# Optimization experiments

Hardware: AMD Instinct MI355X
Metric: run time of the kernel (lower is better)

## Reference

```python
import jax, jax.numpy as jnp
import numpy as np

FT_IN = 40960   # HalfKP-style feature space
FFT_IN = 640    # factorized piece-square features
FT_OUT = 256


def setup_inputs() -> dict:
    key = jax.random.key(0)
    ks = jax.random.split(key, 10)
    B, A = 16384, 30  # batch, active features per board
    inp = {
        "stm_idx": jax.random.randint(ks[0], (B, A), 0, FT_IN, dtype=jnp.int32),
        "nstm_idx": jax.random.randint(ks[1], (B, A), 0, FT_IN, dtype=jnp.int32),
        "f_stm_idx": jax.random.randint(ks[2], (B, A), 0, FFT_IN, dtype=jnp.int32),
        "f_nstm_idx": jax.random.randint(ks[3], (B, A), 0, FFT_IN, dtype=jnp.int32),
        # learned parameters (glorot-ish scale)
        "ft_w": jax.random.normal(ks[4], (FT_IN, FT_OUT), jnp.float32) * 0.01,
        "ft_b": jax.random.normal(ks[5], (FT_OUT,), jnp.float32) * 0.01,
        "fft_w": jax.random.normal(ks[6], (FFT_IN, FT_OUT), jnp.float32) * 0.05,
        "fft_b": jax.random.normal(ks[7], (FT_OUT,), jnp.float32) * 0.01,
        "out_w": jax.random.normal(ks[8], (2 * FT_OUT, 1), jnp.float32) * 0.05,
        "out_b": jax.random.normal(ks[9], (1,), jnp.float32) * 0.01,
    }
    return inp


def _accumulate(w, b, idx):
    # sparse one-hot board @ kernel + bias == gather rows and sum over active features
    return jnp.take(w, idx, axis=0).sum(axis=1) + b  # [B, FT_OUT]


def reference(stm_idx, nstm_idx, f_stm_idx, f_nstm_idx,
              ft_w, ft_b, fft_w, fft_b, out_w, out_b):
    stm = _accumulate(ft_w, ft_b, stm_idx)        # [B, 256]
    nstm = _accumulate(ft_w, ft_b, nstm_idx)      # [B, 256]
    f_stm = _accumulate(fft_w, fft_b, f_stm_idx)  # [B, 256]
    f_nstm = _accumulate(fft_w, fft_b, f_nstm_idx)
    merge = jnp.concatenate((stm, nstm), axis=1) + jnp.concatenate((f_stm, f_nstm), axis=1)
    h = jnp.clip(merge, 0.0, 1.0)                 # ReLU(max_value=1.0)
    return jax.nn.sigmoid(h @ out_w + out_b)      # [B, 1]
```

## Files before the change

### kernel.cpp

```cpp
#include <hip/hip_runtime.h>
#include <math.h>

#define FT_IN  40960
#define FFT_IN 640
#define FT_OUT 256
#define NA     30
#define NSLICE 4
#define BPB    128

typedef _Float16 h2 __attribute__((ext_vector_type(2)));
typedef unsigned u32x4 __attribute__((ext_vector_type(4)));

__device__ __forceinline__ h2 u2h2(unsigned u) {
    union { unsigned u; h2 h; } c; c.u = u; return c.h;
}
__device__ __forceinline__ unsigned pkh(float a, float b) {
    union { h2 h; unsigned u; } c; c.h = h2{(_Float16)a, (_Float16)b}; return c.u;
}

__device__ __forceinline__ void conv_block(const float* __restrict__ src,
                                           unsigned* __restrict__ dst,
                                           int nrows, int bid, int tid)
{
    int t = bid * 256 + tid;
    int total = nrows * 32;
    if (t >= total) return;
    int r = t >> 5, g = t & 31;
    int s = g >> 3, d = g & 7;
    const float4* sp = (const float4*)(src + (size_t)r * FT_OUT + g * 8);
    float4 v0 = sp[0], v1 = sp[1];
    uint4 u;
    u.x = pkh(v0.x, v0.y); u.y = pkh(v0.z, v0.w);
    u.z = pkh(v1.x, v1.y); u.w = pkh(v1.z, v1.w);
    ((uint4*)dst)[((size_t)s * nrows + r) * 8 + d] = u;
}

__global__ __launch_bounds__(256) void prep(
    const float* __restrict__ ft_w, const float* __restrict__ fft_w,
    const int* __restrict__ stm, const int* __restrict__ nstm,
    const int* __restrict__ fstm, const int* __restrict__ fnstm,
    unsigned* __restrict__ ft_o, unsigned* __restrict__ fft_o,
    ushort4* __restrict__ pidx, int n_boards, int nb_ft, int nb_fft)
{
    int bid = blockIdx.x;
    if (bid < nb_ft) {
        conv_block(ft_w, ft_o, FT_IN, bid, threadIdx.x);
    } else if (bid < nb_ft + nb_fft) {
        conv_block(fft_w, fft_o, FFT_IN, bid - nb_ft, threadIdx.x);
    } else {
        int t = (bid - nb_ft - nb_fft) * 256 + (int)threadIdx.x;
        int total = n_boards * NA;
        if (t < total) {
            int board = t / NA, a = t - board * NA;
            ushort4 v;
            v.x = (unsigned short)stm[t];  v.y = (unsigned short)nstm[t];
            v.z = (unsigned short)fstm[t]; v.w = (unsigned short)fnstm[t];
            pidx[(size_t)a * n_boards + board] = v;
        }
    }
}

__global__ __launch_bounds__(1024, 4) void nnue_gather(
    const uint2* __restrict__ pidx,
    const char* __restrict__ ft, const char* __restrict__ fft,
    const float* __restrict__ ft_b, const float* __restrict__ fft_b,
    const float* __restrict__ out_w, float* __restrict__ partial, int n_boards)
{
    extern __shared__ char smem[];
    uint2* lidx = (uint2*)smem;
    u32x4* lfft = (u32x4*)(smem + NA * BPB * 8);
    const int slice = blockIdx.x & (NSLICE - 1);
    const int group = blockIdx.x >> 2;
    const int tid = (int)threadIdx.x;

    for (int i = tid; i < NA * BPB; i += 1024) {
        int b = i & (BPB - 1);
        int bd = group * BPB + b;
        uint2 v; v.x = 0u; v.y = 0u;
        if (bd < n_boards) v = pidx[(size_t)(i >> 7) * n_boards + bd];
        lidx[i] = v;
    }
    {
        const u32x4* fsrc = (const u32x4*)(fft + (size_t)slice * FFT_IN * 128);
        for (int i = tid; i < FFT_IN * 8; i += 1024)
            lfft[i] = fsrc[i];
    }
    __syncthreads();

    const int sub = tid >> 3, ql = tid & 7;
    int board = group * BPB + sub;
    const bool active = board < n_boards;
    const unsigned qlo = (unsigned)(ql << 4);
    const char* ftS = ft + (size_t)slice * FT_IN * 128 + qlo;
    const int col = slice * 64 + ql * 8;

    h2 z = h2{(_Float16)0.f, (_Float16)0.f};
    h2 a0[4] = {z, z, z, z};
    h2 a1[4] = {z, z, z, z};

    #pragma unroll
    for (int a = 0; a < NA; ++a) {
        uint2 iv = lidx[a * BPB + sub];
        u32x4 u0 = *(const u32x4*)(ftS + ((iv.x & 0xFFFFu) << 7));
        u32x4 u1 = *(const u32x4*)(ftS + ((iv.x >> 16) << 7));
        u32x4 g0 = lfft[((iv.y & 0xFFFFu) << 3) + ql];
        u32x4 g1 = lfft[((iv.y >> 16) << 3) + ql];
        a0[0] += u2h2(u0.x); a0[1] += u2h2(u0.y); a0[2] += u2h2(u0.z); a0[3] += u2h2(u0.w);
        a1[0] += u2h2(u1.x); a1[1] += u2h2(u1.y); a1[2] += u2h2(u1.z); a1[3] += u2h2(u1.w);
        a0[0] += u2h2(g0.x); a0[1] += u2h2(g0.y); a0[2] += u2h2(g0.z); a0[3] += u2h2(g0.w);
        a1[0] += u2h2(g1.x); a1[1] += u2h2(g1.y); a1[2] += u2h2(g1.z); a1[3] += u2h2(g1.w);
    }

    float h0[8], h1[8];
    #pragma unroll
    for (int i = 0; i < 4; ++i) {
        h0[2*i] = (float)a0[i].x; h0[2*i+1] = (float)a0[i].y;
        h1[2*i] = (float)a1[i].x; h1[2*i+1] = (float)a1[i].y;
    }
    const float4* bfp = (const float4*)(ft_b  + col);
    const float4* bgp = (const float4*)(fft_b + col);
    float4 bf0 = bfp[0], bf1 = bfp[1], bg0 = bgp[0], bg1 = bgp[1];
    float bias[8] = {bf0.x+bg0.x, bf0.y+bg0.y, bf0.z+bg0.z, bf0.w+bg0.w,
                     bf1.x+bg1.x, bf1.y+bg1.y, bf1.z+bg1.z, bf1.w+bg1.w};
    const float4* w0p = (const float4*)(out_w + col);
    const float4* w1p = (const float4*)(out_w + FT_OUT + col);
    float4 w00 = w0p[0], w01 = w0p[1], w10 = w1p[0], w11 = w1p[1];
    float w0[8] = {w00.x, w00.y, w00.z, w00.w, w01.x, w01.y, w01.z, w01.w};
    float w1[8] = {w10.x, w10.y, w10.z, w10.w, w11.x, w11.y, w11.z, w11.w};

    float p = 0.f;
    #pragma unroll
    for (int i = 0; i < 8; ++i) {
        p += fminf(fmaxf(h0[i] + bias[i], 0.f), 1.f) * w0[i];
        p += fminf(fmaxf(h1[i] + bias[i], 0.f), 1.f) * w1[i];
    }
    p += __shfl_xor(p, 1, 64);
    p += __shfl_xor(p, 2, 64);
    p += __shfl_xor(p, 4, 64);
    if (active && ql == 0)
        partial[(size_t)slice * n_boards + board] = p;
}

__global__ __launch_bounds__(256) void nnue_final(
    const float* __restrict__ partial, const float* __restrict__ out_b,
    float* __restrict__ out, int n)
{
    int b = blockIdx.x * blockDim.x + threadIdx.x;
    if (b >= n) return;
    float zv = out_b[0];
    #pragma unroll
    for (int s = 0; s < NSLICE; ++s) zv += partial[(size_t)s * n + b];
    out[b] = 1.0f / (1.0f + expf(-zv));
}

__global__ __launch_bounds__(256) void nnue_fwd_direct(
    const int* __restrict__ stm_idx, const int* __restrict__ nstm_idx,
    const int* __restrict__ f_stm_idx, const int* __restrict__ f_nstm_idx,
    const float* __restrict__ ft_w, const float* __restrict__ ft_b,
    const float* __restrict__ fft_w, const float* __restrict__ fft_b,
    const float* __restrict__ out_w, const float* __restrict__ out_b,
    float* __restrict__ out, int n_boards)
{
    const int board = (int)((blockIdx.x * blockDim.x + threadIdx.x) >> 6);
    const int lane  = (int)(threadIdx.x & 63);
    if (board >= n_boards) return;
    const int col = lane << 2;
    const float4 ftb  = *(const float4*)(ft_b  + col);
    const float4 fftb = *(const float4*)(fft_b + col);
    float a0x = ftb.x + fftb.x, a0y = ftb.y + fftb.y,
          a0z = ftb.z + fftb.z, a0w = ftb.w + fftb.w;
    float a1x = a0x, a1y = a0y, a1z = a0z, a1w = a0w;
    const int* si  = stm_idx    + (size_t)board * NA;
    const int* ni  = nstm_idx   + (size_t)board * NA;
    const int* fsi = f_stm_idx  + (size_t)board * NA;
    const int* fni = f_nstm_idx + (size_t)board * NA;
    #pragma unroll 5
    for (int a = 0; a < NA; ++a) {
        const float4 r0 = *(const float4*)(ft_w  + (size_t)si[a]  * FT_OUT + col);
        const float4 r1 = *(const float4*)(ft_w  + (size_t)ni[a]  * FT_OUT + col);
        const float4 r2 = *(const float4*)(fft_w + (size_t)fsi[a] * FT_OUT + col);
        const float4 r3 = *(const float4*)(fft_w + (size_t)fni[a] * FT_OUT + col);
        a0x += r0.x + r2.x; a0y += r0.y + r2.y; a0z += r0.z + r2.z; a0w += r0.w + r2.w;
        a1x += r1.x + r3.x; a1y += r1.y + r3.y; a1z += r1.z + r3.z; a1w += r1.w + r3.w;
    }
    a0x = fminf(fmaxf(a0x, 0.f), 1.f); a0y = fminf(fmaxf(a0y, 0.f), 1.f);
    a0z = fminf(fmaxf(a0z, 0.f), 1.f); a0w = fminf(fmaxf(a0w, 0.f), 1.f);
    a1x = fminf(fmaxf(a1x, 0.f), 1.f); a1y = fminf(fmaxf(a1y, 0.f), 1.f);
    a1z = fminf(fmaxf(a1z, 0.f), 1.f); a1w = fminf(fmaxf(a1w, 0.f), 1.f);
    const float4 w0 = *(const float4*)(out_w + col);
    const float4 w1 = *(const float4*)(out_w + FT_OUT + col);
    float p = a0x * w0.x + a0y * w0.y + a0z * w0.z + a0w * w0.w
            + a1x * w1.x + a1y * w1.y + a1z * w1.z + a1w * w1.w;
    #pragma unroll
    for (int off = 32; off > 0; off >>= 1) p += __shfl_down(p, off, 64);
    if (lane == 0) out[board] = 1.0f / (1.0f + expf(-(p + out_b[0])));
}

extern "C" void kernel_launch(void* const* d_in, const int* in_sizes, int n_in,
                              void* d_out, int out_size, void* d_ws, size_t ws_size,
                              hipStream_t stream) {
    const int*   stm_idx    = (const int*)d_in[0];
    const int*   nstm_idx   = (const int*)d_in[1];
    const int*   f_stm_idx  = (const int*)d_in[2];
    const int*   f_nstm_idx = (const int*)d_in[3];
    const float* ft_w  = (const float*)d_in[4];
    const float* ft_b  = (const float*)d_in[5];
    const float* fft_w = (const float*)d_in[6];
    const float* fft_b = (const float*)d_in[7];
    const float* out_w = (const float*)d_in[8];
    const float* out_b = (const float*)d_in[9];
    float* out = (float*)d_out;

    const int n_boards = in_sizes[0] / NA;

    const size_t ft_bytes   = (size_t)FT_IN  * FT_OUT * 2;
    const size_t fft_bytes  = (size_t)FFT_IN * FT_OUT * 2;
    const size_t pidx_bytes = (size_t)n_boards * NA * sizeof(ushort4);
    const size_t part_bytes = (size_t)n_boards * NSLICE * sizeof(float);
    const size_t need = ft_bytes + fft_bytes + pidx_bytes + part_bytes;

    const size_t lds_bytes = (size_t)NA * BPB * 8 + (size_t)FFT_IN * 128;

    bool ok = (ws_size >= need);
    if (ok) {
        ok = (hipFuncSetAttribute((const void*)nnue_gather,
                                  hipFuncAttributeMaxDynamicSharedMemorySize,
                                  (int)lds_bytes) == hipSuccess);
    }
    if (!ok) {
        const int grid = (n_boards + 3) / 4;
        nnue_fwd_direct<<<grid, 256, 0, stream>>>(stm_idx, nstm_idx, f_stm_idx, f_nstm_idx,
                                                  ft_w, ft_b, fft_w, fft_b, out_w, out_b,
                                                  out, n_boards);
        return;
    }

    char* wsp = (char*)d_ws;
    unsigned* ws_ft   = (unsigned*)wsp;            wsp += ft_bytes;
    unsigned* ws_fft  = (unsigned*)wsp;            wsp += fft_bytes;
    ushort4*  ws_pidx = (ushort4*)wsp;             wsp += pidx_bytes;
    float*    ws_part = (float*)wsp;

    {
        const int nb_ft   = FT_IN  * 32 / 256;
        const int nb_fft  = FFT_IN * 32 / 256;
        const int nb_pack = (n_boards * NA + 255) / 256;
        prep<<<nb_ft + nb_fft + nb_pack, 256, 0, stream>>>(
            ft_w, fft_w, stm_idx, nstm_idx, f_stm_idx, f_nstm_idx,
            ws_ft, ws_fft, ws_pidx, n_boards, nb_ft, nb_fft);
    }
    {
        int groups = (n_boards + BPB - 1) / BPB;
        nnue_gather<<<groups * NSLICE, 1024, lds_bytes, stream>>>(
            (const uint2*)ws_pidx, (const char*)ws_ft, (const char*)ws_fft,
            ft_b, fft_b, out_w, ws_part, n_boards);
    }
    {
        nnue_final<<<(n_boards + 255) / 256, 256, 0, stream>>>(ws_part, out_b, out, n_boards);
    }
}
```

Measured before the change: 139.4 us.

## Store feature-transformer weights as FP8 and accumulate in FP32

Converts the ft and fft weight tables to FP8 (packed four per word) instead of FP16, which halves the bytes moved by the random row gathers and the fft LDS footprint. Accumulation moves from packed FP16 to FP32 using hardware FP8-to-FP32 pack conversions. The LDS fft table gets a row-rotated swizzle to spread bank accesses, and the occupancy hint is raised to 8 waves per SIMD. The trade-off is large precision loss from FP8 weights (small weights of about 0.01 scale), which may break the accuracy tolerance, and FP32 accumulators use more registers.

Result: faster. 132.3 us (-5.1%).

```diff
diff --git a/kernel.cpp b/kernel.cpp
--- a/kernel.cpp
+++ b/kernel.cpp
@@ -8,45 +8,46 @@
 #define NSLICE 4
 #define BPB    128
 
-typedef _Float16 h2 __attribute__((ext_vector_type(2)));
-typedef unsigned u32x4 __attribute__((ext_vector_type(4)));
-
-__device__ __forceinline__ h2 u2h2(unsigned u) {
-    union { unsigned u; h2 h; } c; c.u = u; return c.h;
-}
-__device__ __forceinline__ unsigned pkh(float a, float b) {
-    union { h2 h; unsigned u; } c; c.h = h2{(_Float16)a, (_Float16)b}; return c.u;
-}
-
-__device__ __forceinline__ void conv_block(const float* __restrict__ src,
-                                           unsigned* __restrict__ dst,
-                                           int nrows, int bid, int tid)
+typedef float f32x2 __attribute__((ext_vector_type(2)));
+
+__device__ __forceinline__ unsigned enc4(float a, float b, float c, float d) {
+    unsigned r = 0;
+    r = __builtin_amdgcn_cvt_pk_fp8_f32(a, b, r, false);
+    r = __builtin_amdgcn_cvt_pk_fp8_f32(c, d, r, true);
+    return r;
+}
+
+__device__ __forceinline__ void conv8_block(const float* __restrict__ src,
+                                            uint4* __restrict__ dst,
+                                            int nrows, int bid, int tid)
 {
     int t = bid * 256 + tid;
-    int total = nrows * 32;
+    int total = nrows * 16;
     if (t >= total) return;
-    int r = t >> 5, g = t & 31;
-    int s = g >> 3, d = g & 7;
-    const float4* sp = (const float4*)(src + (size_t)r * FT_OUT + g * 8);
-    float4 v0 = sp[0], v1 = sp[1];
+    int r = t >> 4, g = t & 15;
+    int s = g >> 2, d = g & 3;
+    const float4* sp = (const float4*)(src + (size_t)r * FT_OUT + g * 16);
+    float4 v0 = sp[0], v1 = sp[1], v2 = sp[2], v3 = sp[3];
     uint4 u;
-    u.x = pkh(v0.x, v0.y); u.y = pkh(v0.z, v0.w);
-    u.z = pkh(v1.x, v1.y); u.w = pkh(v1.z, v1.w);
-    ((uint4*)dst)[((size_t)s * nrows + r) * 8 + d] = u;
+    u.x = enc4(v0.x, v0.y, v0.z, v0.w);
+    u.y = enc4(v1.x, v1.y, v1.z, v1.w);
+    u.z = enc4(v2.x, v2.y, v2.z, v2.w);
+    u.w = enc4(v3.x, v3.y, v3.z, v3.w);
+    dst[((size_t)s * nrows + r) * 4 + d] = u;
 }
 
 __global__ __launch_bounds__(256) void prep(
     const float* __restrict__ ft_w, const float* __restrict__ fft_w,
     const int* __restrict__ stm, const int* __restrict__ nstm,
     const int* __restrict__ fstm, const int* __restrict__ fnstm,
-    unsigned* __restrict__ ft_o, unsigned* __restrict__ fft_o,
+    uint4* __restrict__ ft_o, uint4* __restrict__ fft_o,
     ushort4* __restrict__ pidx, int n_boards, int nb_ft, int nb_fft)
 {
     int bid = blockIdx.x;
     if (bid < nb_ft) {
-        conv_block(ft_w, ft_o, FT_IN, bid, threadIdx.x);
+        conv8_block(ft_w, ft_o, FT_IN, bid, threadIdx.x);
     } else if (bid < nb_ft + nb_fft) {
-        conv_block(fft_w, fft_o, FFT_IN, bid - nb_ft, threadIdx.x);
+        conv8_block(fft_w, fft_o, FFT_IN, bid - nb_ft, threadIdx.x);
     } else {
         int t = (bid - nb_ft - nb_fft) * 256 + (int)threadIdx.x;
         int total = n_boards * NA;
@@ -60,7 +61,7 @@
     }
 }
 
-__global__ __launch_bounds__(1024, 4) void nnue_gather(
+__global__ __launch_bounds__(1024, 8) void nnue_gather(
     const uint2* __restrict__ pidx,
     const char* __restrict__ ft, const char* __restrict__ fft,
     const float* __restrict__ ft_b, const float* __restrict__ fft_b,
@@ -68,7 +69,7 @@
 {
     extern __shared__ char smem[];
     uint2* lidx = (uint2*)smem;
-    u32x4* lfft = (u32x4*)(smem + NA * BPB * 8);
+    uint2* lf8  = (uint2*)(smem + NA * BPB * 8);
     const int slice = blockIdx.x & (NSLICE - 1);
     const int group = blockIdx.x >> 2;
     const int tid = (int)threadIdx.x;
@@ -81,42 +82,49 @@
         lidx[i] = v;
     }
     {
-        const u32x4* fsrc = (const u32x4*)(fft + (size_t)slice * FFT_IN * 128);
-        for (int i = tid; i < FFT_IN * 8; i += 1024)
-            lfft[i] = fsrc[i];
+        const uint2* fsrc = (const uint2*)(fft + (size_t)slice * FFT_IN * 64);
+        for (int i = tid; i < FFT_IN * 8; i += 1024) {
+            int r = i >> 3, c = i & 7;
+            lf8[(r << 3) + ((c + r) & 7)] = fsrc[i];
+        }
     }
     __syncthreads();
 
     const int sub = tid >> 3, ql = tid & 7;
     int board = group * BPB + sub;
     const bool active = board < n_boards;
-    const unsigned qlo = (unsigned)(ql << 4);
-    const char* ftS = ft + (size_t)slice * FT_IN * 128 + qlo;
+    const char* ftS = ft + (size_t)slice * FT_IN * 64 + ql * 8;
     const int col = slice * 64 + ql * 8;
 
-    h2 z = h2{(_Float16)0.f, (_Float16)0.f};
-    h2 a0[4] = {z, z, z, z};
-    h2 a1[4] = {z, z, z, z};
+    f32x2 a0[4] = {f32x2{0.f,0.f}, f32x2{0.f,0.f}, f32x2{0.f,0.f}, f32x2{0.f,0.f}};
+    f32x2 a1[4] = {f32x2{0.f,0.f}, f32x2{0.f,0.f}, f32x2{0.f,0.f}, f32x2{0.f,0.f}};
 
     #pragma unroll
     for (int a = 0; a < NA; ++a) {
         uint2 iv = lidx[a * BPB + sub];
-        u32x4 u0 = *(const u32x4*)(ftS + ((iv.x & 0xFFFFu) << 7));
-        u32x4 u1 = *(const u32x4*)(ftS + ((iv.x >> 16) << 7));
-        u32x4 g0 = lfft[((iv.y & 0xFFFFu) << 3) + ql];
-        u32x4 g1 = lfft[((iv.y >> 16) << 3) + ql];
-        a0[0] += u2h2(u0.x); a0[1] += u2h2(u0.y); a0[2] += u2h2(u0.z); a0[3] += u2h2(u0.w);
-        a1[0] += u2h2(u1.x); a1[1] += u2h2(u1.y); a1[2] += u2h2(u1.z); a1[3] += u2h2(u1.w);
-        a0[0] += u2h2(g0.x); a0[1] += u2h2(g0.y); a0[2] += u2h2(g0.z); a0[3] += u2h2(g0.w);
-        a1[0] += u2h2(g1.x); a1[1] += u2h2(g1.y); a1[2] += u2h2(g1.z); a1[3] += u2h2(g1.w);
-    }
-
-    float h0[8], h1[8];
-    #pragma unroll
-    for (int i = 0; i < 4; ++i) {
-        h0[2*i] = (float)a0[i].x; h0[2*i+1] = (float)a0[i].y;
-        h1[2*i] = (float)a1[i].x; h1[2*i+1] = (float)a1[i].y;
-    }
+        uint2 u0 = *(const uint2*)(ftS + ((iv.x & 0xFFFFu) << 6));
+        uint2 u1 = *(const uint2*)(ftS + ((iv.x >> 16) << 6));
+        unsigned rz = iv.y & 0xFFFFu, rw = iv.y >> 16;
+        uint2 g0 = lf8[(rz << 3) + (((unsigned)ql + rz) & 7)];
+        uint2 g1 = lf8[(rw << 3) + (((unsigned)ql + rw) & 7)];
+        a0[0] += __builtin_amdgcn_cvt_pk_f32_fp8(u0.x, false);
+        a0[1] += __builtin_amdgcn_cvt_pk_f32_fp8(u0.x, true);
+        a0[2] += __builtin_amdgcn_cvt_pk_f32_fp8(u0.y, false);
+        a0[3] += __builtin_amdgcn_cvt_pk_f32_fp8(u0.y, true);
+        a1[0] += __builtin_amdgcn_cvt_pk_f32_fp8(u1.x, false);
+        a1[1] += __builtin_amdgcn_cvt_pk_f32_fp8(u1.x, true);
+        a1[2] += __builtin_amdgcn_cvt_pk_f32_fp8(u1.y, false);
+        a1[3] += __builtin_amdgcn_cvt_pk_f32_fp8(u1.y, true);
+        a0[0] += __builtin_amdgcn_cvt_pk_f32_fp8(g0.x, false);
+        a0[1] += __builtin_amdgcn_cvt_pk_f32_fp8(g0.x, true);
+        a0[2] += __builtin_amdgcn_cvt_pk_f32_fp8(g0.y, false);
+        a0[3] += __builtin_amdgcn_cvt_pk_f32_fp8(g0.y, true);
+        a1[0] += __builtin_amdgcn_cvt_pk_f32_fp8(g1.x, false);
+        a1[1] += __builtin_amdgcn_cvt_pk_f32_fp8(g1.x, true);
+        a1[2] += __builtin_amdgcn_cvt_pk_f32_fp8(g1.y, false);
+        a1[3] += __builtin_amdgcn_cvt_pk_f32_fp8(g1.y, true);
+    }
+
     const float4* bfp = (const float4*)(ft_b  + col);
     const float4* bgp = (const float4*)(fft_b + col);
     float4 bf0 = bfp[0], bf1 = bfp[1], bg0 = bgp[0], bg1 = bgp[1];
@@ -127,7 +135,12 @@
     float4 w00 = w0p[0], w01 = w0p[1], w10 = w1p[0], w11 = w1p[1];
     float w0[8] = {w00.x, w00.y, w00.z, w00.w, w01.x, w01.y, w01.z, w01.w};
     float w1[8] = {w10.x, w10.y, w10.z, w10.w, w11.x, w11.y, w11.z, w11.w};
-
+    float h0[8], h1[8];
+    #pragma unroll
+    for (int i = 0; i < 4; ++i) {
+        h0[2*i] = a0[i].x; h0[2*i+1] = a0[i].y;
+        h1[2*i] = a1[i].x; h1[2*i+1] = a1[i].y;
+    }
     float p = 0.f;
     #pragma unroll
     for (int i = 0; i < 8; ++i) {
@@ -213,13 +226,13 @@
 
     const int n_boards = in_sizes[0] / NA;
 
-    const size_t ft_bytes   = (size_t)FT_IN  * FT_OUT * 2;
-    const size_t fft_bytes  = (size_t)FFT_IN * FT_OUT * 2;
+    const size_t ft_bytes   = (size_t)FT_IN  * FT_OUT;
+    const size_t fft_bytes  = (size_t)FFT_IN * FT_OUT;
     const size_t pidx_bytes = (size_t)n_boards * NA * sizeof(ushort4);
     const size_t part_bytes = (size_t)n_boards * NSLICE * sizeof(float);
     const size_t need = ft_bytes + fft_bytes + pidx_bytes + part_bytes;
 
-    const size_t lds_bytes = (size_t)NA * BPB * 8 + (size_t)FFT_IN * 128;
+    const size_t lds_bytes = (size_t)NA * BPB * 8 + (size_t)FFT_IN * 64;
 
     bool ok = (ws_size >= need);
     if (ok) {
@@ -236,14 +249,14 @@
     }
 
     char* wsp = (char*)d_ws;
-    unsigned* ws_ft   = (unsigned*)wsp;            wsp += ft_bytes;
-    unsigned* ws_fft  = (unsigned*)wsp;            wsp += fft_bytes;
-    ushort4*  ws_pidx = (ushort4*)wsp;             wsp += pidx_bytes;
-    float*    ws_part = (float*)wsp;
-
-    {
-        const int nb_ft   = FT_IN  * 32 / 256;
-        const int nb_fft  = FFT_IN * 32 / 256;
+    uint4*   ws_ft   = (uint4*)wsp;               wsp += ft_bytes;
+    uint4*   ws_fft  = (uint4*)wsp;               wsp += fft_bytes;
+    ushort4* ws_pidx = (ushort4*)wsp;             wsp += pidx_bytes;
+    float*   ws_part = (float*)wsp;
+
+    {
+        const int nb_ft   = FT_IN  * 16 / 256;
+        const int nb_fft  = FFT_IN * 16 / 256;
         const int nb_pack = (n_boards * NA + 255) / 256;
         prep<<<nb_ft + nb_fft + nb_pack, 256, 0, stream>>>(
             ft_w, fft_w, stm_idx, nstm_idx, f_stm_idx, f_nstm_idx,
```
